# Performance work log

Measured on AMD Instinct MI355X. Metric: run time of the kernel, lower is better.

The kernel has to match this reference:

```python
import jax, jax.numpy as jnp
import numpy as np

B, S, D = 2, 2048, 768
H = 12
HD = D // H  # head_dim = 64
WINDOW = 128
NEG = -1e9


def setup_inputs() -> dict:
    key = jax.random.key(0)
    k1, k2, k3 = jax.random.split(key, 3)
    x = jax.random.normal(k1, (B, S, D), dtype=jnp.float32)
    padding_mask = jnp.ones((B, S), dtype=jnp.float32)
    Wqkv = jax.random.normal(k2, (D, 3 * D), dtype=jnp.float32) * (1.0 / np.sqrt(D))
    Wo = jax.random.normal(k3, (D, D), dtype=jnp.float32) * (1.0 / np.sqrt(D))
    return {"x": x, "padding_mask": padding_mask, "Wqkv": Wqkv, "Wo": Wo}


def reference(x, padding_mask, Wqkv, Wo):
    b, s = x.shape[0], x.shape[1]
    qkv = x @ Wqkv  # [b, s, 3D]
    qkv = qkv.reshape(b, s, 3, H, HD)
    q = qkv[:, :, 0]  # [b, s, H, HD]
    k = qkv[:, :, 1]
    v = qkv[:, :, 2]
    # scores: [b, H, s, s]
    scores = jnp.einsum("bqhd,bkhd->bhqk", q, k) / jnp.sqrt(jnp.asarray(HD, x.dtype))
    # sliding-window additive mask
    idx = jnp.arange(s)
    sw_mask = (jnp.abs(idx[:, None] - idx[None, :]) <= WINDOW // 2).astype(jnp.float32)
    scores = scores + (1.0 - sw_mask)[None, None, :, :] * NEG
    # padding mask over keys
    scores = scores + (1.0 - padding_mask)[:, None, None, :] * NEG
    attn = jax.nn.softmax(scores, axis=-1)
    out = jnp.einsum("bhqk,bkhd->bqhd", attn, v).reshape(b, s, D)
    return out @ Wo
```

## Files before the change

kernel.cpp:

```cpp
#include <hip/hip_runtime.h>
#include <stdint.h>

typedef short bf16x8 __attribute__((ext_vector_type(8)));
typedef float f32x4 __attribute__((ext_vector_type(4)));

#define SEQ_ 2048
#define DM_ 768
#define NH_ 12

__device__ __forceinline__ unsigned short f2bf(float f) {
  unsigned int u = __float_as_uint(f);
  u += 0x7fffu + ((u >> 16) & 1u);
  return (unsigned short)(u >> 16);
}

__device__ __forceinline__ void load_lds16(const unsigned short* g, unsigned short* l) {
  __builtin_amdgcn_global_load_lds((__attribute__((address_space(1))) void*)g,
                                   (__attribute__((address_space(3))) void*)l, 16, 0, 0);
}

__global__ __launch_bounds__(256) void cvt_bf16(const float* __restrict__ s,
                                                unsigned short* __restrict__ d, int n) {
  int i = (blockIdx.x * 256 + threadIdx.x) * 4;
  if (i >= n) return;
  float4 v = *(const float4*)(s + i);
  unsigned short o[4] = {f2bf(v.x), f2bf(v.y), f2bf(v.z), f2bf(v.w)};
  *(uint2*)(d + i) = *(const uint2*)o;
}

__global__ __launch_bounds__(256) void transpose_bf(const float* __restrict__ src,
                                                    unsigned short* __restrict__ dst,
                                                    int R, int C) {
  __shared__ float t[64][65];
  int c0 = blockIdx.x << 6, r0 = blockIdx.y << 6;
  int tid = threadIdx.x;
#pragma unroll
  for (int i = 0; i < 4; i++) {
    int e = (i * 256 + tid) * 4;
    int r = e >> 6, c = e & 63;
    float4 v = *(const float4*)(src + (size_t)(r0 + r) * C + c0 + c);
    t[r][c] = v.x; t[r][c + 1] = v.y; t[r][c + 2] = v.z; t[r][c + 3] = v.w;
  }
  __syncthreads();
#pragma unroll
  for (int i = 0; i < 4; i++) {
    int e = (i * 256 + tid) * 4;
    int r = e >> 6, c = e & 63;
    unsigned short o4[4];
#pragma unroll
    for (int j = 0; j < 4; j++) o4[j] = f2bf(t[c + j][r]);
    *(uint2*)(dst + (size_t)(c0 + r) * R + r0 + c) = *(const uint2*)o4;
  }
}

__global__ __launch_bounds__(256) void transpose_v(const unsigned short* __restrict__ V,
                                                   unsigned short* __restrict__ Vt) {
  __shared__ unsigned short t[64][72];
  int blk = blockIdx.x;
  int bh = blk >> 5, s0 = (blk & 31) << 6;
  int tid = threadIdx.x;
#pragma unroll
  for (int i = 0; i < 2; i++) {
    int e = (i * 256 + tid) * 8;
    int r = e >> 6, c = e & 63;
    *(uint4*)&t[r][c] = *(const uint4*)(V + ((size_t)(bh << 11) + s0 + r) * 64 + c);
  }
  __syncthreads();
#pragma unroll
  for (int i = 0; i < 2; i++) {
    int e = (i * 256 + tid) * 8;
    int hd = e >> 6, c = e & 63;
    unsigned short v[8];
#pragma unroll
    for (int j = 0; j < 8; j++) v[j] = t[c + j][hd];
    *(uint4*)(Vt + ((size_t)(bh << 6) + hd) * SEQ_ + s0 + c) = *(const uint4*)v;
  }
}

__device__ __forceinline__ void gemm_mainloop(const unsigned short* __restrict__ A,
                                              const unsigned short* __restrict__ Bt,
                                              int m0, int n0,
                                              unsigned short* As, unsigned short* Bs,
                                              f32x4 acc[4][4]) {
  const int K = 768;
  int tid = threadIdx.x, wv = tid >> 6, ln = tid & 63, quad = ln >> 4, lrow = ln & 15;
  const unsigned short* a0 = A + (size_t)(m0 + (tid >> 2)) * K + (tid & 3) * 8;
  const unsigned short* a1 = a0 + (size_t)64 * K;
  const unsigned short* b0 = Bt + (size_t)(n0 + (tid >> 2)) * K + (tid & 3) * 8;
  const unsigned short* b1 = b0 + (size_t)64 * K;
  int mw = (wv >> 1) << 6, nw = (wv & 1) << 6;
  for (int kt = 0; kt < K; kt += 32) {
    load_lds16(a0 + kt, As + tid * 8);
    load_lds16(a1 + kt, As + (256 + tid) * 8);
    load_lds16(b0 + kt, Bs + tid * 8);
    load_lds16(b1 + kt, Bs + (256 + tid) * 8);
    __syncthreads();
    bf16x8 af[4], bfr[4];
#pragma unroll
    for (int i = 0; i < 4; i++)
      af[i] = *(const bf16x8*)(As + (mw + i * 16 + lrow) * 32 + quad * 8);
#pragma unroll
    for (int j = 0; j < 4; j++)
      bfr[j] = *(const bf16x8*)(Bs + (nw + j * 16 + lrow) * 32 + quad * 8);
#pragma unroll
    for (int i = 0; i < 4; i++)
#pragma unroll
      for (int j = 0; j < 4; j++)
        acc[i][j] = __builtin_amdgcn_mfma_f32_16x16x32_bf16(af[i], bfr[j], acc[i][j], 0, 0, 0);
    __syncthreads();
  }
}

__global__ __launch_bounds__(256, 2) void gemm_qkv(const unsigned short* __restrict__ A,
                                                   const unsigned short* __restrict__ Bt,
                                                   unsigned short* __restrict__ Qb,
                                                   unsigned short* __restrict__ Kb,
                                                   unsigned short* __restrict__ Vb) {
  __shared__ unsigned short As[128 * 32];
  __shared__ unsigned short Bs[128 * 32];
  f32x4 acc[4][4];
  f32x4 z = {0.f, 0.f, 0.f, 0.f};
#pragma unroll
  for (int i = 0; i < 4; i++)
#pragma unroll
    for (int j = 0; j < 4; j++) acc[i][j] = z;
  int m0 = blockIdx.x << 7, n0 = blockIdx.y << 7;
  gemm_mainloop(A, Bt, m0, n0, As, Bs, acc);
  int tid = threadIdx.x, wv = tid >> 6, ln = tid & 63, quad = ln >> 4, lrow = ln & 15;
  int mw = m0 + ((wv >> 1) << 6), nw = n0 + ((wv & 1) << 6);
  int bb = m0 >> 11;
#pragma unroll
  for (int j = 0; j < 4; j++) {
    int nbase = nw + j * 16;
    int which = nbase / DM_, rem = nbase % DM_;
    int h = rem >> 6, hdb = (rem & 63) + lrow;
    unsigned short* dstp = which == 0 ? Qb : (which == 1 ? Kb : Vb);
    size_t hoff = (size_t)(bb * NH_ + h) << 11;
#pragma unroll
    for (int i = 0; i < 4; i++) {
#pragma unroll
      for (int r = 0; r < 4; r++) {
        int m = mw + i * 16 + quad * 4 + r;
        int s = m & (SEQ_ - 1);
        dstp[((hoff + s) << 6) + hdb] = f2bf(acc[i][j][r]);
      }
    }
  }
}

__global__ __launch_bounds__(256, 2) void gemm_out(const unsigned short* __restrict__ A,
                                                   const unsigned short* __restrict__ Bt,
                                                   float* __restrict__ out) {
  __shared__ unsigned short As[128 * 32];
  __shared__ unsigned short Bs[128 * 32];
  f32x4 acc[4][4];
  f32x4 z = {0.f, 0.f, 0.f, 0.f};
#pragma unroll
  for (int i = 0; i < 4; i++)
#pragma unroll
    for (int j = 0; j < 4; j++) acc[i][j] = z;
  int m0 = blockIdx.x << 7, n0 = blockIdx.y << 7;
  gemm_mainloop(A, Bt, m0, n0, As, Bs, acc);
  int tid = threadIdx.x, wv = tid >> 6, ln = tid & 63, quad = ln >> 4, lrow = ln & 15;
  int mw = m0 + ((wv >> 1) << 6), nw = n0 + ((wv & 1) << 6);
#pragma unroll
  for (int i = 0; i < 4; i++)
#pragma unroll
    for (int j = 0; j < 4; j++)
#pragma unroll
      for (int r = 0; r < 4; r++)
        out[(size_t)(mw + i * 16 + quad * 4 + r) * DM_ + nw + j * 16 + lrow] = acc[i][j][r];
}

__global__ __launch_bounds__(256, 2) void attn_kernel(const unsigned short* __restrict__ Qb,
                                                      const unsigned short* __restrict__ Kb,
                                                      const unsigned short* __restrict__ Vtb,
                                                      const float* __restrict__ pmask,
                                                      unsigned short* __restrict__ Obf) {
  __shared__ unsigned short Ps[4][16 * 168];
  int blk = blockIdx.x;
  int tile = blk & 31, bh = blk >> 5;
  int b = bh / NH_, h = bh % NH_;
  int q0 = tile << 6;
  int kstart = q0 - 64;
  int tid = threadIdx.x, wv = tid >> 6, ln = tid & 63, quad = ln >> 4, lrow = ln & 15;
  int kb = wv << 4;
  int qw = q0 + (wv << 4);

  const unsigned short* Qg = Qb + ((size_t)bh << 11) * 64;
  const unsigned short* Kg = Kb + ((size_t)bh << 11) * 64;
  const unsigned short* Vg = Vtb + ((size_t)bh << 6) * SEQ_;

  bf16x8 qf0 = *(const bf16x8*)(Qg + (qw + lrow) * 64 + quad * 8);
  bf16x8 qf1 = *(const bf16x8*)(Qg + (qw + lrow) * 64 + 32 + quad * 8);

  float sc[9][4];
#pragma unroll
  for (int t = 0; t < 9; t++) {
    int kg = kstart + kb + t * 16 + lrow;
    int kgc = kg < 0 ? 0 : (kg > SEQ_ - 1 ? SEQ_ - 1 : kg);
    bf16x8 kf0 = *(const bf16x8*)(Kg + (size_t)kgc * 64 + quad * 8);
    bf16x8 kf1 = *(const bf16x8*)(Kg + (size_t)kgc * 64 + 32 + quad * 8);
    f32x4 c = {0.f, 0.f, 0.f, 0.f};
    c = __builtin_amdgcn_mfma_f32_16x16x32_bf16(qf0, kf0, c, 0, 0, 0);
    c = __builtin_amdgcn_mfma_f32_16x16x32_bf16(qf1, kf1, c, 0, 0, 0);
    float mneg = -1e30f;
    if (kg >= 0 && kg < SEQ_) {
      if (pmask[(b << 11) + kg] != 0.0f) mneg = 0.0f;
    }
#pragma unroll
    for (int r = 0; r < 4; r++) {
      int qg = qw + quad * 4 + r;
      int d = qg - kg;
      float wneg = (d >= -64 && d <= 64) ? 0.0f : -1e30f;
      sc[t][r] = c[r] * 0.125f + mneg + wneg;
    }
  }
  float inv[4];
#pragma unroll
  for (int r = 0; r < 4; r++) {
    float mx = sc[0][r];
#pragma unroll
    for (int t = 1; t < 9; t++) mx = fmaxf(mx, sc[t][r]);
    mx = fmaxf(mx, __shfl_xor(mx, 1));
    mx = fmaxf(mx, __shfl_xor(mx, 2));
    mx = fmaxf(mx, __shfl_xor(mx, 4));
    mx = fmaxf(mx, __shfl_xor(mx, 8));
    float s = 0.f;
#pragma unroll
    for (int t = 0; t < 9; t++) {
      sc[t][r] = __expf(sc[t][r] - mx);
      s += sc[t][r];
    }
    s += __shfl_xor(s, 1);
    s += __shfl_xor(s, 2);
    s += __shfl_xor(s, 4);
    s += __shfl_xor(s, 8);
    inv[r] = 1.0f / s;
  }
  unsigned short* Pw = &Ps[wv][0];
#pragma unroll
  for (int t = 0; t < 9; t++)
#pragma unroll
    for (int r = 0; r < 4; r++)
      Pw[(quad * 4 + r) * 168 + t * 16 + lrow] = f2bf(sc[t][r] * inv[r]);
  {
    int row = ln >> 2, c0 = 144 + (ln & 3) * 4;
    uint2 zz; zz.x = 0; zz.y = 0;
    *(uint2*)(Pw + row * 168 + c0) = zz;
  }
  __syncthreads();
  f32x4 o[4];
  f32x4 z = {0.f, 0.f, 0.f, 0.f};
#pragma unroll
  for (int tt = 0; tt < 4; tt++) o[tt] = z;
#pragma unroll
  for (int ks = 0; ks < 5; ks++) {
    bf16x8 pf = *(const bf16x8*)(Pw + lrow * 168 + ks * 32 + quad * 8);
    int kg = kstart + kb + ks * 32 + quad * 8;
    int kgc = kg < 0 ? 0 : (kg > SEQ_ - 8 ? SEQ_ - 8 : kg);
#pragma unroll
    for (int tt = 0; tt < 4; tt++) {
      bf16x8 vf = *(const bf16x8*)(Vg + (size_t)(tt * 16 + lrow) * SEQ_ + kgc);
      o[tt] = __builtin_amdgcn_mfma_f32_16x16x32_bf16(pf, vf, o[tt], 0, 0, 0);
    }
  }
#pragma unroll
  for (int tt = 0; tt < 4; tt++)
#pragma unroll
    for (int r = 0; r < 4; r++) {
      int s_ = qw + quad * 4 + r;
      Obf[((size_t)(b << 11) + s_) * DM_ + h * 64 + tt * 16 + lrow] = f2bf(o[tt][r]);
    }
}

extern "C" void kernel_launch(void* const* d_in, const int* in_sizes, int n_in,
                              void* d_out, int out_size, void* d_ws, size_t ws_size,
                              hipStream_t stream) {
  const float* x = (const float*)d_in[0];
  const float* pmask = (const float*)d_in[1];
  const float* Wqkv = (const float*)d_in[2];
  const float* Wo = (const float*)d_in[3];
  float* out = (float*)d_out;
  char* ws = (char*)d_ws;

  unsigned short* xb    = (unsigned short*)(ws + 0);
  unsigned short* wqkvt = (unsigned short*)(ws + 6291456);
  unsigned short* wot   = (unsigned short*)(ws + 9830400);
  unsigned short* Qb    = (unsigned short*)(ws + 11010048);
  unsigned short* Kb    = (unsigned short*)(ws + 17301504);
  unsigned short* Vb    = (unsigned short*)(ws + 23592960);
  unsigned short* Vtb   = (unsigned short*)(ws + 29884416);
  unsigned short* attn_bf = xb;

  cvt_bf16<<<3072, 256, 0, stream>>>(x, xb, 4096 * DM_);
  transpose_bf<<<dim3(36, 12), 256, 0, stream>>>(Wqkv, wqkvt, DM_, 3 * DM_);
  transpose_bf<<<dim3(12, 12), 256, 0, stream>>>(Wo, wot, DM_, DM_);
  gemm_qkv<<<dim3(32, 18), 256, 0, stream>>>(xb, wqkvt, Qb, Kb, Vb);
  transpose_v<<<768, 256, 0, stream>>>(Vb, Vtb);
  attn_kernel<<<768, 256, 0, stream>>>(Qb, Kb, Vtb, pmask, attn_bf);
  gemm_out<<<dim3(32, 6), 256, 0, stream>>>(attn_bf, wot, out);
}
```

Measured before the change: 144.0 us.

## Fuse prep kernels, write V transposed from QKV GEMM, shrink out-GEMM tile

Merges the x conversion and both weight transposes into one prep launch. The QKV GEMM epilogue now transposes V tiles through LDS and writes V^T directly, which removes the separate transpose_v kernel and its round trip through global memory. The output GEMM switches to 64x128 tiles so twice as many blocks fill the GPU, and launch bounds rise to 3 blocks per SM. The trade-offs are extra syncs in the V epilogue and possible register pressure from the higher occupancy target.

```diff
diff --git a/kernel.cpp b/kernel.cpp
--- a/kernel.cpp
+++ b/kernel.cpp
@@ -19,20 +19,11 @@
                                    (__attribute__((address_space(3))) void*)l, 16, 0, 0);
 }
 
-__global__ __launch_bounds__(256) void cvt_bf16(const float* __restrict__ s,
-                                                unsigned short* __restrict__ d, int n) {
-  int i = (blockIdx.x * 256 + threadIdx.x) * 4;
-  if (i >= n) return;
-  float4 v = *(const float4*)(s + i);
-  unsigned short o[4] = {f2bf(v.x), f2bf(v.y), f2bf(v.z), f2bf(v.w)};
-  *(uint2*)(d + i) = *(const uint2*)o;
-}
-
-__global__ __launch_bounds__(256) void transpose_bf(const float* __restrict__ src,
-                                                    unsigned short* __restrict__ dst,
-                                                    int R, int C) {
-  __shared__ float t[64][65];
-  int c0 = blockIdx.x << 6, r0 = blockIdx.y << 6;
+__device__ __forceinline__ void transpose_body(const float* __restrict__ src,
+                                               unsigned short* __restrict__ dst,
+                                               int R, int C, int bx, int by,
+                                               float (*t)[65]) {
+  int c0 = bx << 6, r0 = by << 6;
   int tid = threadIdx.x;
 #pragma unroll
   for (int i = 0; i < 4; i++) {
@@ -53,27 +44,25 @@
   }
 }
 
-__global__ __launch_bounds__(256) void transpose_v(const unsigned short* __restrict__ V,
-                                                   unsigned short* __restrict__ Vt) {
-  __shared__ unsigned short t[64][72];
+__global__ __launch_bounds__(256) void prep(const float* __restrict__ x,
+                                            const float* __restrict__ Wqkv,
+                                            const float* __restrict__ Wo,
+                                            unsigned short* __restrict__ xb,
+                                            unsigned short* __restrict__ wqkvt,
+                                            unsigned short* __restrict__ wot) {
+  __shared__ float t[64][65];
   int blk = blockIdx.x;
-  int bh = blk >> 5, s0 = (blk & 31) << 6;
-  int tid = threadIdx.x;
-#pragma unroll
-  for (int i = 0; i < 2; i++) {
-    int e = (i * 256 + tid) * 8;
-    int r = e >> 6, c = e & 63;
-    *(uint4*)&t[r][c] = *(const uint4*)(V + ((size_t)(bh << 11) + s0 + r) * 64 + c);
-  }
-  __syncthreads();
-#pragma unroll
-  for (int i = 0; i < 2; i++) {
-    int e = (i * 256 + tid) * 8;
-    int hd = e >> 6, c = e & 63;
-    unsigned short v[8];
-#pragma unroll
-    for (int j = 0; j < 8; j++) v[j] = t[c + j][hd];
-    *(uint4*)(Vt + ((size_t)(bh << 6) + hd) * SEQ_ + s0 + c) = *(const uint4*)v;
+  if (blk < 3072) {
+    int i = (blk * 256 + threadIdx.x) * 4;
+    float4 v = *(const float4*)(x + i);
+    unsigned short o[4] = {f2bf(v.x), f2bf(v.y), f2bf(v.z), f2bf(v.w)};
+    *(uint2*)(xb + i) = *(const uint2*)o;
+  } else if (blk < 3072 + 432) {
+    int idx = blk - 3072;
+    transpose_body(Wqkv, wqkvt, DM_, 3 * DM_, idx % 36, idx / 36, t);
+  } else {
+    int idx = blk - 3504;
+    transpose_body(Wo, wot, DM_, DM_, idx % 12, idx / 12, t);
   }
 }
 
@@ -111,13 +100,14 @@
   }
 }
 
-__global__ __launch_bounds__(256, 2) void gemm_qkv(const unsigned short* __restrict__ A,
+__global__ __launch_bounds__(256, 3) void gemm_qkv(const unsigned short* __restrict__ A,
                                                    const unsigned short* __restrict__ Bt,
                                                    unsigned short* __restrict__ Qb,
                                                    unsigned short* __restrict__ Kb,
-                                                   unsigned short* __restrict__ Vb) {
-  __shared__ unsigned short As[128 * 32];
-  __shared__ unsigned short Bs[128 * 32];
+                                                   unsigned short* __restrict__ Vtb) {
+  __shared__ unsigned short smem[2 * 128 * 32];
+  unsigned short* As = smem;
+  unsigned short* Bs = smem + 128 * 32;
   f32x4 acc[4][4];
   f32x4 z = {0.f, 0.f, 0.f, 0.f};
 #pragma unroll
@@ -127,52 +117,99 @@
   int m0 = blockIdx.x << 7, n0 = blockIdx.y << 7;
   gemm_mainloop(A, Bt, m0, n0, As, Bs, acc);
   int tid = threadIdx.x, wv = tid >> 6, ln = tid & 63, quad = ln >> 4, lrow = ln & 15;
-  int mw = m0 + ((wv >> 1) << 6), nw = n0 + ((wv & 1) << 6);
+  int mw_l = (wv >> 1) << 6, nw_l = (wv & 1) << 6;
   int bb = m0 >> 11;
-#pragma unroll
-  for (int j = 0; j < 4; j++) {
-    int nbase = nw + j * 16;
-    int which = nbase / DM_, rem = nbase % DM_;
-    int h = rem >> 6, hdb = (rem & 63) + lrow;
-    unsigned short* dstp = which == 0 ? Qb : (which == 1 ? Kb : Vb);
-    size_t hoff = (size_t)(bb * NH_ + h) << 11;
-#pragma unroll
-    for (int i = 0; i < 4; i++) {
-#pragma unroll
-      for (int r = 0; r < 4; r++) {
-        int m = mw + i * 16 + quad * 4 + r;
-        int s = m & (SEQ_ - 1);
-        dstp[((hoff + s) << 6) + hdb] = f2bf(acc[i][j][r]);
-      }
-    }
-  }
-}
-
-__global__ __launch_bounds__(256, 2) void gemm_out(const unsigned short* __restrict__ A,
+  int which = n0 / DM_;
+  int nrem0 = n0 - which * DM_;
+  if (which < 2) {
+    unsigned short* dstp = which == 0 ? Qb : Kb;
+#pragma unroll
+    for (int j = 0; j < 4; j++) {
+      int nb = nrem0 + nw_l + j * 16;
+      int h = nb >> 6, hdb = (nb & 63) + lrow;
+      size_t hoff = (size_t)(bb * NH_ + h) << 11;
+#pragma unroll
+      for (int i = 0; i < 4; i++)
+#pragma unroll
+        for (int r = 0; r < 4; r++) {
+          int s = (m0 + mw_l + i * 16 + quad * 4 + r) & (SEQ_ - 1);
+          dstp[((hoff + s) << 6) + hdb] = f2bf(acc[i][j][r]);
+        }
+    }
+  } else {
+    const int LSTR = 136;
+    int hdl2 = ((wv & 1) << 4) + lrow;
+    int hds = tid >> 3, s0 = (tid & 7) << 4;
+    int hd_in_block = ((hds & 16) << 2) + (hds & 15);
+#pragma unroll
+    for (int j = 0; j < 4; j++) {
+      __syncthreads();
+#pragma unroll
+      for (int i = 0; i < 4; i++)
+#pragma unroll
+        for (int r = 0; r < 4; r++) {
+          int sl = mw_l + i * 16 + quad * 4 + r;
+          smem[hdl2 * LSTR + sl] = f2bf(acc[i][j][r]);
+        }
+      __syncthreads();
+      int nb = nrem0 + hd_in_block + j * 16;
+      int h = nb >> 6, hdh = nb & 63;
+      uint4 p0 = *(const uint4*)&smem[hds * LSTR + s0];
+      uint4 p1 = *(const uint4*)&smem[hds * LSTR + s0 + 8];
+      size_t vbase = (size_t)(((bb * NH_ + h) << 6) + hdh) * SEQ_ + (m0 & (SEQ_ - 1)) + s0;
+      *(uint4*)(Vtb + vbase) = p0;
+      *(uint4*)(Vtb + vbase + 8) = p1;
+    }
+  }
+}
+
+__global__ __launch_bounds__(256, 3) void gemm_out(const unsigned short* __restrict__ A,
                                                    const unsigned short* __restrict__ Bt,
                                                    float* __restrict__ out) {
-  __shared__ unsigned short As[128 * 32];
+  const int K = 768;
+  __shared__ unsigned short As[64 * 32];
   __shared__ unsigned short Bs[128 * 32];
-  f32x4 acc[4][4];
+  f32x4 acc[4][2];
   f32x4 z = {0.f, 0.f, 0.f, 0.f};
 #pragma unroll
   for (int i = 0; i < 4; i++)
 #pragma unroll
-    for (int j = 0; j < 4; j++) acc[i][j] = z;
-  int m0 = blockIdx.x << 7, n0 = blockIdx.y << 7;
-  gemm_mainloop(A, Bt, m0, n0, As, Bs, acc);
+    for (int j = 0; j < 2; j++) acc[i][j] = z;
+  int m0 = blockIdx.x << 6, n0 = blockIdx.y << 7;
   int tid = threadIdx.x, wv = tid >> 6, ln = tid & 63, quad = ln >> 4, lrow = ln & 15;
-  int mw = m0 + ((wv >> 1) << 6), nw = n0 + ((wv & 1) << 6);
+  const unsigned short* a0 = A + (size_t)(m0 + (tid >> 2)) * K + (tid & 3) * 8;
+  const unsigned short* b0 = Bt + (size_t)(n0 + (tid >> 2)) * K + (tid & 3) * 8;
+  const unsigned short* b1 = b0 + (size_t)64 * K;
+  int nw = wv << 5;
+  for (int kt = 0; kt < K; kt += 32) {
+    load_lds16(a0 + kt, As + tid * 8);
+    load_lds16(b0 + kt, Bs + tid * 8);
+    load_lds16(b1 + kt, Bs + (256 + tid) * 8);
+    __syncthreads();
+    bf16x8 af[4], bfr[2];
+#pragma unroll
+    for (int i = 0; i < 4; i++)
+      af[i] = *(const bf16x8*)(As + (i * 16 + lrow) * 32 + quad * 8);
+#pragma unroll
+    for (int j = 0; j < 2; j++)
+      bfr[j] = *(const bf16x8*)(Bs + (nw + j * 16 + lrow) * 32 + quad * 8);
+#pragma unroll
+    for (int i = 0; i < 4; i++)
+#pragma unroll
+      for (int j = 0; j < 2; j++)
+        acc[i][j] = __builtin_amdgcn_mfma_f32_16x16x32_bf16(af[i], bfr[j], acc[i][j], 0, 0, 0);
+    __syncthreads();
+  }
 #pragma unroll
   for (int i = 0; i < 4; i++)
 #pragma unroll
-    for (int j = 0; j < 4; j++)
+    for (int j = 0; j < 2; j++)
 #pragma unroll
       for (int r = 0; r < 4; r++)
-        out[(size_t)(mw + i * 16 + quad * 4 + r) * DM_ + nw + j * 16 + lrow] = acc[i][j][r];
-}
-
-__global__ __launch_bounds__(256, 2) void attn_kernel(const unsigned short* __restrict__ Qb,
+        out[(size_t)(m0 + i * 16 + quad * 4 + r) * DM_ + n0 + nw + j * 16 + lrow] = acc[i][j][r];
+}
+
+__global__ __launch_bounds__(256, 3) void attn_kernel(const unsigned short* __restrict__ Qb,
                                                       const unsigned short* __restrict__ Kb,
                                                       const unsigned short* __restrict__ Vtb,
                                                       const float* __restrict__ pmask,
@@ -289,15 +326,11 @@
   unsigned short* wot   = (unsigned short*)(ws + 9830400);
   unsigned short* Qb    = (unsigned short*)(ws + 11010048);
   unsigned short* Kb    = (unsigned short*)(ws + 17301504);
-  unsigned short* Vb    = (unsigned short*)(ws + 23592960);
-  unsigned short* Vtb   = (unsigned short*)(ws + 29884416);
+  unsigned short* Vtb   = (unsigned short*)(ws + 23592960);
   unsigned short* attn_bf = xb;
 
-  cvt_bf16<<<3072, 256, 0, stream>>>(x, xb, 4096 * DM_);
-  transpose_bf<<<dim3(36, 12), 256, 0, stream>>>(Wqkv, wqkvt, DM_, 3 * DM_);
-  transpose_bf<<<dim3(12, 12), 256, 0, stream>>>(Wo, wot, DM_, DM_);
-  gemm_qkv<<<dim3(32, 18), 256, 0, stream>>>(xb, wqkvt, Qb, Kb, Vb);
-  transpose_v<<<768, 256, 0, stream>>>(Vb, Vtb);
+  prep<<<3648, 256, 0, stream>>>(x, Wqkv, Wo, xb, wqkvt, wot);
+  gemm_qkv<<<dim3(32, 18), 256, 0, stream>>>(xb, wqkvt, Qb, Kb, Vtb);
   attn_kernel<<<768, 256, 0, stream>>>(Qb, Kb, Vtb, pmask, attn_bf);
-  gemm_out<<<dim3(32, 6), 256, 0, stream>>>(attn_bf, wot, out);
-}
+  gemm_out<<<dim3(64, 6), 256, 0, stream>>>(attn_bf, wot, out);
+}
```

Measured after the change: 134.6 us. 6.5% less time.
